# Optimization experiments

Hardware: AMD Instinct MI355X
Metric: run time of the kernel (lower is better)

## Reference

```python
import jax, jax.numpy as jnp
import numpy as np

P, Q = 3, 3          # degrees
M, N = 127, 127      # max span index per direction (ctrl grid is (M+1)x(N+1))
DIM = 3
SU, SV = 256, 256    # out_dim_u, out_dim_v
B = 16
EPS = 1e-08


def _normalize_knots(knots):
    # cumsum of positive increments, rescaled to [0, 1]
    kc = jnp.cumsum(jnp.where(knots < 0.0, 0.0001, knots), axis=1)
    return (kc - kc[:, :1]) / (kc[:, -1:] - kc[:, :1])


def _find_spans(t, K, deg, max_span):
    # t: [S], K: [B, LK] -> spans [B, S] (first interior knot with t - K > EPS, else 1 sentinel)
    d = t[None, None, :] - K[:, deg:-deg, None]          # [B, L_int, S]
    masked = jnp.where(d > EPS, d, 1.0)
    return jnp.clip(jnp.argmin(masked, axis=1) + deg, deg, max_span)


def _basis(t, K, span, deg):
    # Cox-de Boor recursion. t: [S], K: [B, LK], span: [B, S] int -> [B, deg+1, S]
    Bsz, S = span.shape
    tb = t[None, :]
    Ni = [jnp.zeros((Bsz, S), K.dtype) for _ in range(deg + 1)]
    Ni[0] = jnp.ones((Bsz, S), K.dtype)
    for k in range(1, deg + 1):
        saved = jnp.zeros((Bsz, S), K.dtype)
        for r in range(k):
            K1 = jnp.take_along_axis(K, span + r + 1, axis=1)       # [B, S]
            K2 = jnp.take_along_axis(K, span + 1 - k + r, axis=1)   # [B, S]
            denom = (K1 - tb) + (tb - K2)
            temp = jnp.where(denom == 0.0, 0.0001,
                             Ni[r] / jnp.where(denom == 0.0, 1.0, denom))
            Ni[r] = saved + (K1 - tb) * temp
            saved = (tb - K2) * temp
        Ni[k] = saved
    return jnp.stack(Ni, axis=1)


def setup_inputs() -> dict:
    key = jax.random.key(0)
    k1, k2, k3 = jax.random.split(key, 3)
    ctrl_pts = jax.random.normal(k1, (B, M + 1, N + 1, DIM), dtype=jnp.float32)
    knot_u = jax.random.uniform(k2, (B, M + P + 2), dtype=jnp.float32)
    knot_v = jax.random.uniform(k3, (B, N + Q + 2), dtype=jnp.float32)
    u = jnp.linspace(1e-05, 1.0 - 1e-05, SU, dtype=jnp.float32)
    v = jnp.linspace(1e-05, 1.0 - 1e-05, SV, dtype=jnp.float32)
    return {"ctrl_pts": ctrl_pts, "knot_u": knot_u, "knot_v": knot_v, "u": u, "v": v}


def reference(ctrl_pts, knot_u, knot_v, u, v):
    U = _normalize_knots(knot_u)   # [B, M+P+2]
    V = _normalize_knots(knot_v)
    uspan = _find_spans(u, U, P, M)   # [B, SU] int
    vspan = _find_spans(v, V, Q, N)   # [B, SV] int
    Nu = _basis(u, U, uspan, P)       # [B, P+1, SU]
    Nv = _basis(v, V, vspan, Q)       # [B, Q+1, SV]
    # gather control points: pts[b,l,r,i,j,:] = ctrl_pts[b, uspan[b,i]-P+l, vspan[b,j]-Q+r, :]
    u_idx = uspan[:, None, :] - P + jnp.arange(P + 1)[None, :, None]  # [B, P+1, SU]
    v_idx = vspan[:, None, :] - Q + jnp.arange(Q + 1)[None, :, None]  # [B, Q+1, SV]
    b_idx = jnp.arange(B)[:, None, None, None, None]
    pts = ctrl_pts[b_idx,
                   u_idx[:, :, None, :, None],
                   v_idx[:, None, :, None, :], :]  # [B, P+1, Q+1, SU, SV, DIM]
    surfaces = jnp.einsum('bpquvd,bpu,bqv->buvd', pts, Nu, Nv)
    return surfaces[..., :DIM]
```

## Files before the change

### kernel.cpp

```cpp
#include <hip/hip_runtime.h>

#define BATCH 16
#define PDEG  3
#define MAXSPAN 127
#define KLEN  132
#define NSAMP 256
#define NSPANS 126
#define GRID_PTS 128

__device__ float g_N[2][BATCH][NSAMP][4];
__device__ int   g_span[2][BATCH][NSAMP];

__global__ void basis_kernel(const float* __restrict__ knots,
                             const float* __restrict__ t_arr,
                             int axis, int max_span)
{
    __shared__ double s_w[KLEN];
    __shared__ double s_kn[KLEN];
    const int b   = blockIdx.x;
    const int tid = threadIdx.x;

    if (tid < KLEN) {
        float w = knots[b * KLEN + tid];
        s_w[tid] = (w < 0.0f) ? 1.0e-4 : (double)w;
    }
    __syncthreads();

    if (tid == 0) {
        double run = 0.0;
        for (int j = 0; j < KLEN; ++j) { run += s_w[j]; s_kn[j] = run; }
    }
    __syncthreads();

    const double k0  = s_kn[0];
    const double inv = 1.0 / (s_kn[KLEN - 1] - k0);
    double mykn = 0.0;
    if (tid < KLEN) mykn = (s_kn[tid] - k0) * inv;
    __syncthreads();
    if (tid < KLEN) s_kn[tid] = mykn;
    __syncthreads();

    const double t = (double)t_arr[tid];

    double best = 1.0e300;
    int jmin = 0;
    for (int j = 0; j < NSPANS; ++j) {
        double d = t - s_kn[j + PDEG];
        double m = (d > 1.0e-8) ? d : 1.0;
        if (m < best) { best = m; jmin = j; }
    }
    int span = jmin + PDEG;
    if (span > max_span) span = max_span;

    double Ni[PDEG + 1];
    Ni[0] = 1.0;
    for (int k = 1; k <= PDEG; ++k) {
        double saved = 0.0;
        for (int r = 0; r < k; ++r) {
            double K1 = s_kn[span + r + 1];
            double K2 = s_kn[span + 1 - k + r];
            double denom = (K1 - t) + (t - K2);
            double temp = (denom == 0.0) ? 1.0e-4 : (Ni[r] / denom);
            Ni[r] = saved + (K1 - t) * temp;
            saved = (t - K2) * temp;
        }
        Ni[k] = saved;
    }

#pragma unroll
    for (int r = 0; r < 4; ++r)
        g_N[axis][b][tid][r] = (float)Ni[r];
    g_span[axis][b][tid] = span;
}

__global__ void eval_kernel(const float* __restrict__ ctrl,
                            float* __restrict__ out)
{
    const int sv = threadIdx.x;
    const int su = blockIdx.x;
    const int b  = blockIdx.y;

    const int us = g_span[0][b][su];
    const int vs = g_span[1][b][sv];
    const float4 nu4 = *(const float4*)&g_N[0][b][su][0];
    const float4 nv4 = *(const float4*)&g_N[1][b][sv][0];
    const float nu[4] = {nu4.x, nu4.y, nu4.z, nu4.w};
    const float nv[4] = {nv4.x, nv4.y, nv4.z, nv4.w};

    const float* __restrict__ base =
        ctrl + (size_t)b * GRID_PTS * GRID_PTS * 3;

    float acc0 = 0.f, acc1 = 0.f, acc2 = 0.f;
#pragma unroll
    for (int p = 0; p < 4; ++p) {
        const float* __restrict__ row =
            base + ((size_t)(us - PDEG + p) * GRID_PTS + (vs - PDEG)) * 3;
        const float wu = nu[p];
#pragma unroll
        for (int q = 0; q < 4; ++q) {
            const float w = wu * nv[q];
            acc0 += w * row[q * 3 + 0];
            acc1 += w * row[q * 3 + 1];
            acc2 += w * row[q * 3 + 2];
        }
    }

    const size_t o = (((size_t)b * NSAMP + su) * NSAMP + sv) * 3;
    out[o + 0] = acc0;
    out[o + 1] = acc1;
    out[o + 2] = acc2;
}

extern "C" void kernel_launch(void* const* d_in, const int* in_sizes, int n_in,
                              void* d_out, int out_size, void* d_ws, size_t ws_size,
                              hipStream_t stream) {
    const float* ctrl   = (const float*)d_in[0];
    const float* knot_u = (const float*)d_in[1];
    const float* knot_v = (const float*)d_in[2];
    const float* u      = (const float*)d_in[3];
    const float* v      = (const float*)d_in[4];
    float* out = (float*)d_out;

    basis_kernel<<<BATCH, NSAMP, 0, stream>>>(knot_u, u, 0, MAXSPAN);
    basis_kernel<<<BATCH, NSAMP, 0, stream>>>(knot_v, v, 1, MAXSPAN);

    dim3 grid(NSAMP, BATCH);
    eval_kernel<<<grid, NSAMP, 0, stream>>>(ctrl, out);
}
```

Baseline: 86.21 us.

## Merge basis launches, parallel-scan knots, stage control rows in shared memory

The two basis kernels are merged into one launch over a (batch, axis) grid, which removes one kernel launch. The serial single-thread cumsum becomes a Hillis-Steele parallel scan in shared memory. The eval kernel cooperatively loads the four control-point rows for its u-span into shared memory with float4 loads and then reads them from LDS, instead of issuing scattered global loads per thread. This adds a block barrier and 6KB of LDS per block.

```diff
diff --git a/kernel.cpp b/kernel.cpp
--- a/kernel.cpp
+++ b/kernel.cpp
@@ -7,30 +7,37 @@
 #define NSAMP 256
 #define NSPANS 126
 #define GRID_PTS 128
+#define ROWF (GRID_PTS * 3)
 
 __device__ float g_N[2][BATCH][NSAMP][4];
 __device__ int   g_span[2][BATCH][NSAMP];
 
-__global__ void basis_kernel(const float* __restrict__ knots,
-                             const float* __restrict__ t_arr,
-                             int axis, int max_span)
+__global__ void basis_kernel(const float* __restrict__ knot_u,
+                             const float* __restrict__ knot_v,
+                             const float* __restrict__ u_arr,
+                             const float* __restrict__ v_arr)
 {
-    __shared__ double s_w[KLEN];
     __shared__ double s_kn[KLEN];
-    const int b   = blockIdx.x;
-    const int tid = threadIdx.x;
+    const int b    = blockIdx.x;
+    const int axis = blockIdx.y;
+    const int tid  = threadIdx.x;
+
+    const float* __restrict__ knots = axis ? knot_v : knot_u;
+    const float* __restrict__ t_arr = axis ? v_arr  : u_arr;
 
     if (tid < KLEN) {
         float w = knots[b * KLEN + tid];
-        s_w[tid] = (w < 0.0f) ? 1.0e-4 : (double)w;
+        s_kn[tid] = (w < 0.0f) ? 1.0e-4 : (double)w;
     }
     __syncthreads();
 
-    if (tid == 0) {
-        double run = 0.0;
-        for (int j = 0; j < KLEN; ++j) { run += s_w[j]; s_kn[j] = run; }
+    for (int off = 1; off < KLEN; off <<= 1) {
+        double add = 0.0;
+        if (tid < KLEN && tid >= off) add = s_kn[tid - off];
+        __syncthreads();
+        if (tid < KLEN) s_kn[tid] += add;
+        __syncthreads();
     }
-    __syncthreads();
 
     const double k0  = s_kn[0];
     const double inv = 1.0 / (s_kn[KLEN - 1] - k0);
@@ -50,7 +57,7 @@
         if (m < best) { best = m; jmin = j; }
     }
     int span = jmin + PDEG;
-    if (span > max_span) span = max_span;
+    if (span > MAXSPAN) span = MAXSPAN;
 
     double Ni[PDEG + 1];
     Ni[0] = 1.0;
@@ -73,35 +80,42 @@
     g_span[axis][b][tid] = span;
 }
 
-__global__ void eval_kernel(const float* __restrict__ ctrl,
-                            float* __restrict__ out)
+__global__ void __launch_bounds__(256)
+eval_kernel(const float* __restrict__ ctrl, float* __restrict__ out)
 {
+    __shared__ float s_rows[4 * ROWF];
     const int sv = threadIdx.x;
     const int su = blockIdx.x;
     const int b  = blockIdx.y;
 
     const int us = g_span[0][b][su];
+
+    const float4* __restrict__ src = (const float4*)
+        (ctrl + ((size_t)b * GRID_PTS + (size_t)(us - PDEG)) * ROWF);
+    float4* dst = (float4*)s_rows;
+    dst[sv] = src[sv];
+    if (sv < 128) dst[256 + sv] = src[256 + sv];
+
     const int vs = g_span[1][b][sv];
     const float4 nu4 = *(const float4*)&g_N[0][b][su][0];
     const float4 nv4 = *(const float4*)&g_N[1][b][sv][0];
     const float nu[4] = {nu4.x, nu4.y, nu4.z, nu4.w};
     const float nv[4] = {nv4.x, nv4.y, nv4.z, nv4.w};
 
-    const float* __restrict__ base =
-        ctrl + (size_t)b * GRID_PTS * GRID_PTS * 3;
+    __syncthreads();
 
+    const int c = (vs - PDEG) * 3;
     float acc0 = 0.f, acc1 = 0.f, acc2 = 0.f;
 #pragma unroll
     for (int p = 0; p < 4; ++p) {
-        const float* __restrict__ row =
-            base + ((size_t)(us - PDEG + p) * GRID_PTS + (vs - PDEG)) * 3;
+        const float* rp = s_rows + p * ROWF + c;
         const float wu = nu[p];
 #pragma unroll
         for (int q = 0; q < 4; ++q) {
             const float w = wu * nv[q];
-            acc0 += w * row[q * 3 + 0];
-            acc1 += w * row[q * 3 + 1];
-            acc2 += w * row[q * 3 + 2];
+            acc0 += w * rp[q * 3 + 0];
+            acc1 += w * rp[q * 3 + 1];
+            acc2 += w * rp[q * 3 + 2];
         }
     }
 
@@ -121,9 +135,9 @@
     const float* v      = (const float*)d_in[4];
     float* out = (float*)d_out;
 
-    basis_kernel<<<BATCH, NSAMP, 0, stream>>>(knot_u, u, 0, MAXSPAN);
-    basis_kernel<<<BATCH, NSAMP, 0, stream>>>(knot_v, v, 1, MAXSPAN);
+    dim3 bgrid(BATCH, 2);
+    basis_kernel<<<bgrid, NSAMP, 0, stream>>>(knot_u, knot_v, u, v);
 
-    dim3 grid(NSAMP, BATCH);
-    eval_kernel<<<grid, NSAMP, 0, stream>>>(ctrl, out);
+    dim3 egrid(NSAMP, BATCH);
+    eval_kernel<<<egrid, NSAMP, 0, stream>>>(ctrl, out);
 }
```

Result: faster. 76.27 us (-11.5%).
